# Kernel tuning notes

Hardware: AMD Instinct MI355X
Metric: run time of the kernel (lower is better)

## Reference

```python
import jax, jax.numpy as jnp
import numpy as np

N_USERS, N_ITEMS = 100000, 50000
N_EDGES, N_PAIRS = 1000000, 500000
D_IN, D_HID, D_OUT = 128, 128, 64
EPS = 1e-12


def _mean_agg(h_src, src, dst, n_dst):
    # gather src features along edges, scatter-sum to dst, divide by in-degree
    msg = h_src[src]                                            # [E, d]
    s = jax.ops.segment_sum(msg, dst, num_segments=n_dst)       # [n_dst, d]
    deg = jax.ops.segment_sum(jnp.ones(src.shape, h_src.dtype), dst, num_segments=n_dst)
    return s / jnp.maximum(deg, 1.0)[:, None]


def _conv(h_src, h_dst, src, dst, n_dst, Wn, bn, Ws, bs):
    # SAGE-mean style ConvLayer: fc_neigh(mean) + fc_self(dst), ReLU, L2 norm
    hn = _mean_agg(h_src, src, dst, n_dst)
    z = hn @ Wn + bn + h_dst @ Ws + bs
    z = jax.nn.relu(z)
    return z / jnp.maximum(jnp.linalg.norm(z, axis=-1, keepdims=True), EPS)


def _l2n(x):
    return x / jnp.maximum(jnp.linalg.norm(x, axis=-1, keepdims=True), EPS)


def setup_inputs() -> dict:
    key = jax.random.key(0)
    ks = jax.random.split(key, 20)
    f = lambda k, shp: (jax.random.normal(k, shp, jnp.float32) * 0.05)
    ri = lambda k, shp, hi: jax.random.randint(k, shp, 0, hi, jnp.int32)
    return {
        'h_user': jax.random.normal(ks[0], (N_USERS, D_IN), jnp.float32),
        'h_item': jax.random.normal(ks[1], (N_ITEMS, D_IN), jnp.float32),
        'Wn01': f(ks[2], (2, 2, D_HID, D_HID)),
        'bn01': f(ks[3], (2, 2, D_HID)),
        'Ws01': f(ks[4], (2, 2, D_HID, D_HID)),
        'bs01': f(ks[5], (2, 2, D_HID)),
        'Wn2': f(ks[6], (2, D_HID, D_OUT)),
        'bn2': f(ks[7], (2, D_OUT)),
        'Ws2': f(ks[8], (2, D_HID, D_OUT)),
        'bs2': f(ks[9], (2, D_OUT)),
        'u2i_src': ri(ks[10], (N_EDGES,), N_USERS),
        'u2i_dst': ri(ks[11], (N_EDGES,), N_ITEMS),
        'i2u_src': ri(ks[12], (N_EDGES,), N_ITEMS),
        'i2u_dst': ri(ks[13], (N_EDGES,), N_USERS),
        'pos_u': ri(ks[14], (N_PAIRS,), N_USERS),
        'pos_i': ri(ks[15], (N_PAIRS,), N_ITEMS),
        'neg_u': ri(ks[16], (N_PAIRS,), N_USERS),
        'neg_i': ri(ks[17], (N_PAIRS,), N_ITEMS),
    }


def reference(h_user, h_item, Wn01, bn01, Ws01, bs01, Wn2, bn2, Ws2, bs2,
              u2i_src, u2i_dst, i2u_src, i2u_dst, pos_u, pos_i, neg_u, neg_i):
    n_users, n_items = h_user.shape[0], h_item.shape[0]
    hu, hi = h_user, h_item
    # layers 0,1: etype 0 = user->item ('rates'), etype 1 = item->user (reverse)
    for l in range(2):
        hi_new = _conv(hu, hi, u2i_src, u2i_dst, n_items,
                       Wn01[l, 0], bn01[l, 0], Ws01[l, 0], bs01[l, 0])
        hu_new = _conv(hi, hu, i2u_src, i2u_dst, n_users,
                       Wn01[l, 1], bn01[l, 1], Ws01[l, 1], bs01[l, 1])
        hu, hi = hu_new, hi_new
    # layer 2: hidden -> out
    hi_new = _conv(hu, hi, u2i_src, u2i_dst, n_items, Wn2[0], bn2[0], Ws2[0], bs2[0])
    hu_new = _conv(hi, hu, i2u_src, i2u_dst, n_users, Wn2[1], bn2[1], Ws2[1], bs2[1])
    hu, hi = hu_new, hi_new
    # CosinePrediction on pos/neg graphs (user -rates-> item edges)
    nu, ni = _l2n(hu), _l2n(hi)
    pos_score = jnp.sum(nu[pos_u] * ni[pos_i], axis=-1)
    neg_score = jnp.sum(nu[neg_u] * ni[neg_i], axis=-1)
    return hu, hi, pos_score, neg_score
```

## Files before the change

kernel.cpp:

```cpp
#include <hip/hip_runtime.h>
#include <hip/hip_bf16.h>

#define NU 100000
#define NI 50000
#define NE 1000000
#define NP 500000

typedef unsigned short u16;
typedef unsigned int u32;
typedef __attribute__((ext_vector_type(8))) short short8;
typedef __attribute__((ext_vector_type(4))) float f32x4;

static __device__ __forceinline__ u16 f2bf(float f) {
    union { float f; u32 u; } x; x.f = f;
    u32 r = x.u + 0x7fff + ((x.u >> 16) & 1);
    return (u16)(r >> 16);
}
static __device__ __forceinline__ float bf2f(u16 h) {
    union { u32 u; float f; } x; x.u = ((u32)h) << 16;
    return x.f;
}

__global__ __launch_bounds__(256) void cvt_kernel(const float* __restrict__ in,
                                                  u16* __restrict__ out, int n8) {
    int i = blockIdx.x * blockDim.x + threadIdx.x;
    if (i >= n8) return;
    float4 a = ((const float4*)in)[2 * i];
    float4 b = ((const float4*)in)[2 * i + 1];
    ushort4 lo = {f2bf(a.x), f2bf(a.y), f2bf(a.z), f2bf(a.w)};
    ushort4 hi = {f2bf(b.x), f2bf(b.y), f2bf(b.z), f2bf(b.w)};
    ((ushort4*)out)[2 * i]     = lo;
    ((ushort4*)out)[2 * i + 1] = hi;
}

__global__ void wtrans_all_kernel(const float* __restrict__ Wn01,
                                  const float* __restrict__ Ws01,
                                  const float* __restrict__ Wn2,
                                  const float* __restrict__ Ws2,
                                  u16* __restrict__ wt) {
    int x = blockIdx.x;
    int k = threadIdx.x;
    const float *Wn, *Ws; int n, N; size_t off_out;
    if (x < 512) {
        int m = x >> 7; n = x & 127; N = 128;
        Wn = Wn01 + m * 16384; Ws = Ws01 + m * 16384;
        off_out = (size_t)m * 128 * 256;
    } else {
        int m = (x - 512) >> 6; n = (x - 512) & 63; N = 64;
        Wn = Wn2 + m * 8192; Ws = Ws2 + m * 8192;
        off_out = (size_t)4 * 128 * 256 + (size_t)m * 64 * 256;
    }
    wt[off_out + (size_t)n * 256 + k]       = f2bf(Wn[(size_t)k * N + n]);
    wt[off_out + (size_t)n * 256 + 128 + k] = f2bf(Ws[(size_t)k * N + n]);
}


__global__ void hist2_kernel(const int* __restrict__ d0, int* __restrict__ deg0,
                             int* __restrict__ rank0,
                             const int* __restrict__ d1, int* __restrict__ deg1,
                             int* __restrict__ rank1, int E) {
    int e = blockIdx.x * blockDim.x + threadIdx.x;
    if (e >= E) return;
    if (blockIdx.y == 0) {
        int d = __builtin_nontemporal_load(&d0[e]);
        int r = atomicAdd(&deg0[d], 1);
        __builtin_nontemporal_store(r, &rank0[e]);
    } else {
        int d = __builtin_nontemporal_load(&d1[e]);
        int r = atomicAdd(&deg1[d], 1);
        __builtin_nontemporal_store(r, &rank1[e]);
    }
}

__global__ void scan_local_kernel(const int* __restrict__ in, int* __restrict__ out,
                                  int* __restrict__ bsum, int n) {
    __shared__ int s[1024];
    int i = blockIdx.x * 1024 + threadIdx.x;
    int v = (i < n) ? in[i] : 0;
    s[threadIdx.x] = v;
    __syncthreads();
    for (int off = 1; off < 1024; off <<= 1) {
        int t = (threadIdx.x >= off) ? s[threadIdx.x - off] : 0;
        __syncthreads();
        s[threadIdx.x] += t;
        __syncthreads();
    }
    if (i < n) out[i] = s[threadIdx.x] - v;
    if (threadIdx.x == 1023) bsum[blockIdx.x] = s[1023];
}

__global__ void scan_bsum_kernel(int* bsum, int nb) {
    __shared__ int s[1024];
    int v = (threadIdx.x < nb) ? bsum[threadIdx.x] : 0;
    s[threadIdx.x] = v;
    __syncthreads();
    for (int off = 1; off < 1024; off <<= 1) {
        int t = (threadIdx.x >= off) ? s[threadIdx.x - off] : 0;
        __syncthreads();
        s[threadIdx.x] += t;
        __syncthreads();
    }
    if (threadIdx.x < nb) bsum[threadIdx.x] = s[threadIdx.x] - v;
}

__global__ void scan_finalize_kernel(int* __restrict__ rs, const int* __restrict__ bsum,
                                     int n, int E) {
    int i = blockIdx.x * 1024 + threadIdx.x;
    if (i < n) rs[i] += bsum[blockIdx.x];
    if (i == 0) rs[n] = E;
}

__global__ void fill2_kernel(const int* __restrict__ s0, const int* __restrict__ d0,
                             const int* __restrict__ r0, const int* __restrict__ rs0,
                             int* __restrict__ csr0,
                             const int* __restrict__ s1, const int* __restrict__ d1,
                             const int* __restrict__ r1, const int* __restrict__ rs1,
                             int* __restrict__ csr1, int E) {
    const int *src, *dst, *rk, *rs; int* csr;
    if (blockIdx.y == 0) { src = s0; dst = d0; rk = r0; rs = rs0; csr = csr0; }
    else                 { src = s1; dst = d1; rk = r1; rs = rs1; csr = csr1; }
    int e = blockIdx.x * blockDim.x + threadIdx.x;
    if (e >= E) return;
    int d = __builtin_nontemporal_load(&dst[e]);
    int r = __builtin_nontemporal_load(&rk[e]);
    int s = __builtin_nontemporal_load(&src[e]);
    csr[rs[d] + r] = s;
}

__global__ __launch_bounds__(256) void agg2_kernel(
    const u16* __restrict__ hu, const u16* __restrict__ hi,
    const int* __restrict__ rs_i, const int* __restrict__ csr_i,
    u16* __restrict__ out_i, int gi,
    const int* __restrict__ rs_u, const int* __restrict__ csr_u,
    u16* __restrict__ out_u) {
    const u16* hsrc; const int *rs, *csr; u16* out; int T, t;
    int bx = blockIdx.x;
    if (bx < gi) { hsrc = hu; rs = rs_i; csr = csr_i; out = out_i; T = NI;
                   t = bx * 4 + (threadIdx.x >> 6); }
    else         { hsrc = hi; rs = rs_u; csr = csr_u; out = out_u; T = NU;
                   t = (bx - gi) * 4 + (threadIdx.x >> 6); }
    if (t >= T) return;
    const int lane = threadIdx.x & 63;
    const int lr   = lane & 15;
    const int sub  = lane >> 4;
    int e0 = rs[t], e1 = rs[t + 1];
    float acc[8] = {};
    int e = e0 + sub;
    for (; e + 12 < e1; e += 16) {
        int s0 = __builtin_nontemporal_load(&csr[e]);
        int s1 = __builtin_nontemporal_load(&csr[e + 4]);
        int s2 = __builtin_nontemporal_load(&csr[e + 8]);
        int s3 = __builtin_nontemporal_load(&csr[e + 12]);
        short8 v0 = *(const short8*)&hsrc[(size_t)s0 * 128 + (lr << 3)];
        short8 v1 = *(const short8*)&hsrc[(size_t)s1 * 128 + (lr << 3)];
        short8 v2 = *(const short8*)&hsrc[(size_t)s2 * 128 + (lr << 3)];
        short8 v3 = *(const short8*)&hsrc[(size_t)s3 * 128 + (lr << 3)];
        #pragma unroll
        for (int q = 0; q < 8; ++q)
            acc[q] += (bf2f((u16)v0[q]) + bf2f((u16)v1[q])) +
                      (bf2f((u16)v2[q]) + bf2f((u16)v3[q]));
    }
    for (; e + 4 < e1; e += 8) {
        int s0 = __builtin_nontemporal_load(&csr[e]);
        int s1 = __builtin_nontemporal_load(&csr[e + 4]);
        short8 v0 = *(const short8*)&hsrc[(size_t)s0 * 128 + (lr << 3)];
        short8 v1 = *(const short8*)&hsrc[(size_t)s1 * 128 + (lr << 3)];
        #pragma unroll
        for (int q = 0; q < 8; ++q)
            acc[q] += bf2f((u16)v0[q]) + bf2f((u16)v1[q]);
    }
    if (e < e1) {
        int s0 = __builtin_nontemporal_load(&csr[e]);
        short8 v0 = *(const short8*)&hsrc[(size_t)s0 * 128 + (lr << 3)];
        #pragma unroll
        for (int q = 0; q < 8; ++q) acc[q] += bf2f((u16)v0[q]);
    }
    #pragma unroll
    for (int q = 0; q < 8; ++q) {
        acc[q] += __shfl_xor(acc[q], 16);
        acc[q] += __shfl_xor(acc[q], 32);
    }
    if (sub == 0) {
        float inv = (e1 > e0) ? 1.f / (float)(e1 - e0) : 0.f;
        short8 o;
        #pragma unroll
        for (int q = 0; q < 8; ++q) o[q] = (short)f2bf(acc[q] * inv);
        __builtin_nontemporal_store(o, (short8*)&out[(size_t)t * 128 + (lr << 3)]);
    }
}

template <int DOUT, bool WRITE_F32>
__global__ __launch_bounds__(256) void conv2_kernel(
    const u16* __restrict__ hn_i, const u16* __restrict__ hd_i,
    const u16* __restrict__ wt_i, const float* __restrict__ bn_i,
    const float* __restrict__ bs_i, float* __restrict__ outf_i,
    u16* __restrict__ outb_i, int ci,
    const u16* __restrict__ hn_u, const u16* __restrict__ hd_u,
    const u16* __restrict__ wt_u, const float* __restrict__ bn_u,
    const float* __restrict__ bs_u, float* __restrict__ outf_u,
    u16* __restrict__ outb_u)
{
    constexpr int NF   = DOUT / 64;
    constexpr int FSTR = (DOUT == 128) ? 132 : 68;
    __shared__ u16 smA[64 * 264];
    __shared__ float psum[4][64];
    __shared__ float sinv[64];
    float* smF = (float*)smA;

    const u16 *hn, *hd, *Wt; const float *bn, *bs; float* outf; u16* outb; int T, t0;
    if ((int)blockIdx.x < ci) {
        hn = hn_i; hd = hd_i; Wt = wt_i; bn = bn_i; bs = bs_i;
        outf = outf_i; outb = outb_i; T = NI; t0 = blockIdx.x * 64;
    } else {
        hn = hn_u; hd = hd_u; Wt = wt_u; bn = bn_u; bs = bs_u;
        outf = outf_u; outb = outb_u; T = NU; t0 = (blockIdx.x - ci) * 64;
    }

    const int tid  = threadIdx.x;
    const int wave = tid >> 6;
    const int lane = tid & 63;
    const int lr   = lane & 15;
    const int lg   = lane >> 4;

    #pragma unroll
    for (int i = 0; i < 8; ++i) {
        int lin = i * 256 + tid;
        int row = lin >> 5;
        int q   = lin & 31;
        int t   = t0 + row; if (t >= T) t = T - 1;
        const u16* srcp = (q < 16) ? &hn[(size_t)t * 128 + (q << 3)]
                                   : &hd[(size_t)t * 128 + ((q - 16) << 3)];
        *(short8*)&smA[row * 264 + (q << 3)] = *(const short8*)srcp;
    }
    __syncthreads();

    const u16* wp[NF];
    float bias[NF];
    #pragma unroll
    for (int ni = 0; ni < NF; ++ni) {
        int col = wave * (16 * NF) + ni * 16 + lr;
        wp[ni] = Wt + (size_t)col * 256;
        bias[ni] = bn[col] + bs[col];
    }

    f32x4 acc[4][NF];
    #pragma unroll
    for (int mi = 0; mi < 4; ++mi)
        #pragma unroll
        for (int ni = 0; ni < NF; ++ni)
            acc[mi][ni] = (f32x4){0.f, 0.f, 0.f, 0.f};

    #pragma unroll
    for (int ks = 0; ks < 8; ++ks) {
        const int kb = ks * 32 + (lg << 3);
        short8 b[NF];
        #pragma unroll
        for (int ni = 0; ni < NF; ++ni) b[ni] = *(const short8*)&wp[ni][kb];
        #pragma unroll
        for (int mi = 0; mi < 4; ++mi) {
            short8 a = *(const short8*)&smA[(mi * 16 + lr) * 264 + kb];
            #pragma unroll
            for (int ni = 0; ni < NF; ++ni)
                acc[mi][ni] = __builtin_amdgcn_mfma_f32_16x16x32_bf16(a, b[ni], acc[mi][ni], 0, 0, 0);
        }
    }
    __syncthreads();

    float rsum[4][4];
    #pragma unroll
    for (int mi = 0; mi < 4; ++mi) {
        #pragma unroll
        for (int j = 0; j < 4; ++j) {
            int rowg = mi * 16 + lg * 4 + j;
            float s = 0.f;
            #pragma unroll
            for (int ni = 0; ni < NF; ++ni) {
                float z = fmaxf(acc[mi][ni][j] + bias[ni], 0.f);
                int colg = wave * (16 * NF) + ni * 16 + lr;
                smF[rowg * FSTR + colg] = z;
                s = fmaf(z, z, s);
            }
            rsum[mi][j] = s;
        }
    }
    #pragma unroll
    for (int m = 1; m < 16; m <<= 1)
        #pragma unroll
        for (int mi = 0; mi < 4; ++mi)
            #pragma unroll
            for (int j = 0; j < 4; ++j)
                rsum[mi][j] += __shfl_xor(rsum[mi][j], m);
    if (lr == 0) {
        #pragma unroll
        for (int mi = 0; mi < 4; ++mi)
            #pragma unroll
            for (int j = 0; j < 4; ++j)
                psum[wave][mi * 16 + lg * 4 + j] = rsum[mi][j];
    }
    __syncthreads();
    if (tid < 64) {
        float n2 = psum[0][tid] + psum[1][tid] + psum[2][tid] + psum[3][tid];
        sinv[tid] = 1.f / fmaxf(sqrtf(n2), 1e-12f);
    }
    __syncthreads();

    constexpr int GPR  = DOUT / 8;
    constexpr int ITER = 64 * GPR / 256;
    #pragma unroll
    for (int i = 0; i < ITER; ++i) {
        int lin = i * 256 + tid;
        int row = lin / GPR, g = lin % GPR;
        int t = t0 + row;
        if (t < T) {
            float inv = sinv[row];
            float4 z0 = *(float4*)&smF[row * FSTR + g * 8];
            float4 z1 = *(float4*)&smF[row * FSTR + g * 8 + 4];
            float o0 = z0.x * inv, o1 = z0.y * inv, o2 = z0.z * inv, o3 = z0.w * inv;
            float o4 = z1.x * inv, o5 = z1.y * inv, o6 = z1.z * inv, o7 = z1.w * inv;
            short8 ob = {(short)f2bf(o0), (short)f2bf(o1), (short)f2bf(o2), (short)f2bf(o3),
                         (short)f2bf(o4), (short)f2bf(o5), (short)f2bf(o6), (short)f2bf(o7)};
            *(short8*)&outb[(size_t)t * DOUT + g * 8] = ob;
            if (WRITE_F32) {
                *(float4*)&outf[(size_t)t * DOUT + g * 8]     = (float4){o0, o1, o2, o3};
                *(float4*)&outf[(size_t)t * DOUT + g * 8 + 4] = (float4){o4, o5, o6, o7};
            }
        }
    }
}

__global__ __launch_bounds__(256) void score2_kernel(
    const u16* __restrict__ hu, const u16* __restrict__ hi,
    const int* __restrict__ pu0, const int* __restrict__ pi0, float* __restrict__ out0,
    const int* __restrict__ pu1, const int* __restrict__ pi1, float* __restrict__ out1,
    int P) {
    const int *pu, *pi; float* out;
    if (blockIdx.y == 0) { pu = pu0; pi = pi0; out = out0; }
    else                 { pu = pu1; pi = pi1; out = out1; }
    int g = threadIdx.x >> 3, l = threadIdx.x & 7;
    int p = blockIdx.x * 32 + g;
    if (p >= P) return;
    int u = __builtin_nontemporal_load(&pu[p]);
    int it = __builtin_nontemporal_load(&pi[p]);
    short8 a = *(const short8*)&hu[(size_t)u * 64 + (l << 3)];
    short8 b = *(const short8*)&hi[(size_t)it * 64 + (l << 3)];
    float d = 0.f, na = 0.f, nb = 0.f;
    #pragma unroll
    for (int q = 0; q < 8; ++q) {
        float x = bf2f((u16)a[q]), y = bf2f((u16)b[q]);
        d  = fmaf(x, y, d);
        na = fmaf(x, x, na);
        nb = fmaf(y, y, nb);
    }
    #pragma unroll
    for (int m = 1; m < 8; m <<= 1) {
        d  += __shfl_xor(d, m);
        na += __shfl_xor(na, m);
        nb += __shfl_xor(nb, m);
    }
    if (l == 0) out[p] = d / (fmaxf(sqrtf(na), 1e-12f) * fmaxf(sqrtf(nb), 1e-12f));
}


extern "C" void kernel_launch(void* const* d_in, const int* in_sizes, int n_in,
                              void* d_out, int out_size, void* d_ws, size_t ws_size,
                              hipStream_t stream) {
    const float* h_user = (const float*)d_in[0];
    const float* h_item = (const float*)d_in[1];
    const float* Wn01   = (const float*)d_in[2];
    const float* bn01   = (const float*)d_in[3];
    const float* Ws01   = (const float*)d_in[4];
    const float* bs01   = (const float*)d_in[5];
    const float* Wn2    = (const float*)d_in[6];
    const float* bn2    = (const float*)d_in[7];
    const float* Ws2    = (const float*)d_in[8];
    const float* bs2    = (const float*)d_in[9];
    const int* u2i_src  = (const int*)d_in[10];
    const int* u2i_dst  = (const int*)d_in[11];
    const int* i2u_src  = (const int*)d_in[12];
    const int* i2u_dst  = (const int*)d_in[13];
    const int* pos_u    = (const int*)d_in[14];
    const int* pos_i    = (const int*)d_in[15];
    const int* neg_u    = (const int*)d_in[16];
    const int* neg_i    = (const int*)d_in[17];

    float* out = (float*)d_out;
    float* out_hu = out;
    float* out_hi = out + (size_t)NU * 64;
    float* out_pos = out + (size_t)NU * 64 + (size_t)NI * 64;
    float* out_neg = out_pos + NP;

    char* ws = (char*)d_ws;
    size_t off = 0;
    auto alloc = [&](size_t bytes) -> void* {
        void* p = ws + off;
        off = (off + bytes + 255) & ~(size_t)255;
        return p;
    };
    u16* hu0b = (u16*)alloc((size_t)NU * 128 * 2);
    u16* hi0b = (u16*)alloc((size_t)NI * 128 * 2);
    u16* hu_b = (u16*)alloc((size_t)NU * 128 * 2);
    u16* hi_b = (u16*)alloc((size_t)NI * 128 * 2);
    u16* hu_a = (u16*)alloc((size_t)NU * 128 * 2);
    u16* hi_a = (u16*)alloc((size_t)NI * 128 * 2);
    u16* agg_i = (u16*)alloc((size_t)NI * 128 * 2);
    u16* agg_u = (u16*)alloc((size_t)NU * 128 * 2);
    u16* hu2b = (u16*)alloc((size_t)NU * 64 * 2);
    u16* hi2b = (u16*)alloc((size_t)NI * 64 * 2);
    u16* wt_all = (u16*)alloc((size_t)(4 * 128 * 256 + 2 * 64 * 256) * 2);
    u16* wt_l0_i = wt_all;
    u16* wt_l0_u = wt_all + 32768;
    u16* wt_l1_i = wt_all + 65536;
    u16* wt_l1_u = wt_all + 98304;
    u16* wt_l2_i = wt_all + 131072;
    u16* wt_l2_u = wt_all + 147456;
    int* csr_u2i = (int*)alloc((size_t)NE * 4);
    int* csr_i2u = (int*)alloc((size_t)NE * 4);
    int* rs_i   = (int*)alloc((size_t)(NI + 1) * 4);
    int* rs_u   = (int*)alloc((size_t)(NU + 1) * 4);
    int* deg    = (int*)alloc((size_t)(NI + NU) * 4);
    int* bsum   = (int*)alloc(1024 * 4);
    int* deg_i = deg, *deg_u = deg + NI;
    int* rank_i = (int*)agg_i;
    int* rank_u = (int*)agg_u;
    (void)ws_size; (void)in_sizes; (void)n_in; (void)out_size;

    const int eblocks = (NE + 255) / 256;

    cvt_kernel<<<(NU * 128 / 8 + 255) / 256, 256, 0, stream>>>(h_user, hu0b, NU * 128 / 8);
    cvt_kernel<<<(NI * 128 / 8 + 255) / 256, 256, 0, stream>>>(h_item, hi0b, NI * 128 / 8);
    wtrans_all_kernel<<<640, 128, 0, stream>>>(Wn01, Ws01, Wn2, Ws2, wt_all);

    hipMemsetAsync(deg, 0, (size_t)(NI + NU) * 4, stream);
    hist2_kernel<<<dim3(eblocks, 2), 256, 0, stream>>>(u2i_dst, deg_i, rank_i,
                                                       i2u_dst, deg_u, rank_u, NE);
    {
        int nb = (NI + 1023) / 1024;
        scan_local_kernel<<<nb, 1024, 0, stream>>>(deg_i, rs_i, bsum, NI);
        scan_bsum_kernel<<<1, 1024, 0, stream>>>(bsum, nb);
        scan_finalize_kernel<<<nb, 1024, 0, stream>>>(rs_i, bsum, NI, NE);
    }
    {
        int nb = (NU + 1023) / 1024;
        scan_local_kernel<<<nb, 1024, 0, stream>>>(deg_u, rs_u, bsum, NU);
        scan_bsum_kernel<<<1, 1024, 0, stream>>>(bsum, nb);
        scan_finalize_kernel<<<nb, 1024, 0, stream>>>(rs_u, bsum, NU, NE);
    }
    fill2_kernel<<<dim3(eblocks, 2), 256, 0, stream>>>(
        u2i_src, u2i_dst, rank_i, rs_i, csr_u2i,
        i2u_src, i2u_dst, rank_u, rs_u, csr_i2u, NE);

    const int gi = (NI + 3) / 4, gu = (NU + 3) / 4;
    const int ci = (NI + 63) / 64, cu = (NU + 63) / 64;

    agg2_kernel<<<gi + gu, 256, 0, stream>>>(hu0b, hi0b, rs_i, csr_u2i, agg_i, gi,
                                             rs_u, csr_i2u, agg_u);
    conv2_kernel<128, false><<<ci + cu, 256, 0, stream>>>(
        agg_i, hi0b, wt_l0_i, bn01 + 0, bs01 + 0, nullptr, hi_b, ci,
        agg_u, hu0b, wt_l0_u, bn01 + 128, bs01 + 128, nullptr, hu_b);
    agg2_kernel<<<gi + gu, 256, 0, stream>>>(hu_b, hi_b, rs_i, csr_u2i, agg_i, gi,
                                             rs_u, csr_i2u, agg_u);
    conv2_kernel<128, false><<<ci + cu, 256, 0, stream>>>(
        agg_i, hi_b, wt_l1_i, bn01 + 256, bs01 + 256, nullptr, hi_a, ci,
        agg_u, hu_b, wt_l1_u, bn01 + 384, bs01 + 384, nullptr, hu_a);
    agg2_kernel<<<gi + gu, 256, 0, stream>>>(hu_a, hi_a, rs_i, csr_u2i, agg_i, gi,
                                             rs_u, csr_i2u, agg_u);
    conv2_kernel<64, true><<<ci + cu, 256, 0, stream>>>(
        agg_i, hi_a, wt_l2_i, bn2 + 0, bs2 + 0, out_hi, hi2b, ci,
        agg_u, hu_a, wt_l2_u, bn2 + 64, bs2 + 64, out_hu, hu2b);

    score2_kernel<<<dim3((NP + 31) / 32, 2), 256, 0, stream>>>(
        hu2b, hi2b, pos_u, pos_i, out_pos, neg_u, neg_i, out_neg, NP);
}
```

Baseline: 569.3 us.

## Project before aggregation in final layer to halve gather width

For the last layer, features are projected first with a combined 128x128 weight (neighbor half and self half), then the 64-wide neighbor projection is mean-aggregated, since mean aggregation commutes with the linear map. This halves the bytes gathered per edge in the third aggregation, at the cost of an extra projection kernel and a separate combine/normalize kernel. The agg grid is also interleaved between item and user blocks, and the two CSR scans are merged into dual-launch kernels to cut launch count.

Result: slower. 581.9 us (+2.2%).

```diff
diff --git a/kernel.cpp b/kernel.cpp
--- a/kernel.cpp
+++ b/kernel.cpp
@@ -5,6 +5,10 @@
 #define NI 50000
 #define NE 1000000
 #define NP 500000
+
+#define GIB 12500
+#define GUB 25000
+#define AGG_GRID 50000
 
 typedef unsigned short u16;
 typedef unsigned int u32;
@@ -40,18 +44,24 @@
                                   u16* __restrict__ wt) {
     int x = blockIdx.x;
     int k = threadIdx.x;
-    const float *Wn, *Ws; int n, N; size_t off_out;
     if (x < 512) {
-        int m = x >> 7; n = x & 127; N = 128;
-        Wn = Wn01 + m * 16384; Ws = Ws01 + m * 16384;
-        off_out = (size_t)m * 128 * 256;
+        int m = x >> 7, n = x & 127;
+        const float* Wn = Wn01 + m * 16384;
+        const float* Ws = Ws01 + m * 16384;
+        size_t o = (size_t)m * 128 * 256;
+        wt[o + (size_t)n * 256 + k]       = f2bf(Wn[(size_t)k * 128 + n]);
+        wt[o + (size_t)n * 256 + 128 + k] = f2bf(Ws[(size_t)k * 128 + n]);
     } else {
-        int m = (x - 512) >> 6; n = (x - 512) & 63; N = 64;
-        Wn = Wn2 + m * 8192; Ws = Ws2 + m * 8192;
-        off_out = (size_t)4 * 128 * 256 + (size_t)m * 64 * 256;
-    }
-    wt[off_out + (size_t)n * 256 + k]       = f2bf(Wn[(size_t)k * N + n]);
-    wt[off_out + (size_t)n * 256 + 128 + k] = f2bf(Ws[(size_t)k * N + n]);
+        int m = (x - 512) >> 7;
+        int n = (x - 512) & 127;
+        size_t o = 131072 + (size_t)m * 16384;
+        float v;
+        if (m == 0) v = (n < 64) ? Wn2[(size_t)k * 64 + n]
+                                 : Ws2[8192 + (size_t)k * 64 + (n - 64)];
+        else        v = (n < 64) ? Wn2[8192 + (size_t)k * 64 + n]
+                                 : Ws2[(size_t)k * 64 + (n - 64)];
+        wt[o + (size_t)n * 128 + k] = f2bf(v);
+    }
 }
 
 
@@ -72,8 +82,13 @@
     }
 }
 
-__global__ void scan_local_kernel(const int* __restrict__ in, int* __restrict__ out,
-                                  int* __restrict__ bsum, int n) {
+__global__ void scan2_local_kernel(const int* __restrict__ in0, int* __restrict__ out0,
+                                   int* __restrict__ bsum0, int n0,
+                                   const int* __restrict__ in1, int* __restrict__ out1,
+                                   int* __restrict__ bsum1, int n1) {
+    const int* in; int *out, *bsum; int n;
+    if (blockIdx.y == 0) { in = in0; out = out0; bsum = bsum0; n = n0; }
+    else                 { in = in1; out = out1; bsum = bsum1; n = n1; }
     __shared__ int s[1024];
     int i = blockIdx.x * 1024 + threadIdx.x;
     int v = (i < n) ? in[i] : 0;
@@ -89,9 +104,12 @@
     if (threadIdx.x == 1023) bsum[blockIdx.x] = s[1023];
 }
 
-__global__ void scan_bsum_kernel(int* bsum, int nb) {
+__global__ void scan2_bsum_kernel(int* b0, int nb0, int* b1, int nb1) {
+    int* bsum; int nb;
+    if (blockIdx.y == 0) { bsum = b0; nb = nb0; }
+    else                 { bsum = b1; nb = nb1; }
     __shared__ int s[1024];
-    int v = (threadIdx.x < nb) ? bsum[threadIdx.x] : 0;
+    int v = ((int)threadIdx.x < nb) ? bsum[threadIdx.x] : 0;
     s[threadIdx.x] = v;
     __syncthreads();
     for (int off = 1; off < 1024; off <<= 1) {
@@ -100,11 +118,15 @@
         s[threadIdx.x] += t;
         __syncthreads();
     }
-    if (threadIdx.x < nb) bsum[threadIdx.x] = s[threadIdx.x] - v;
-}
-
-__global__ void scan_finalize_kernel(int* __restrict__ rs, const int* __restrict__ bsum,
-                                     int n, int E) {
+    if ((int)threadIdx.x < nb) bsum[threadIdx.x] = s[threadIdx.x] - v;
+}
+
+__global__ void scan2_finalize_kernel(int* __restrict__ rs0, const int* __restrict__ b0,
+                                      int n0, int* __restrict__ rs1,
+                                      const int* __restrict__ b1, int n1, int E) {
+    int* rs; const int* bsum; int n;
+    if (blockIdx.y == 0) { rs = rs0; bsum = b0; n = n0; }
+    else                 { rs = rs1; bsum = b1; n = n1; }
     int i = blockIdx.x * 1024 + threadIdx.x;
     if (i < n) rs[i] += bsum[blockIdx.x];
     if (i == 0) rs[n] = E;
@@ -130,15 +152,18 @@
 __global__ __launch_bounds__(256) void agg2_kernel(
     const u16* __restrict__ hu, const u16* __restrict__ hi,
     const int* __restrict__ rs_i, const int* __restrict__ csr_i,
-    u16* __restrict__ out_i, int gi,
+    u16* __restrict__ out_i,
     const int* __restrict__ rs_u, const int* __restrict__ csr_u,
     u16* __restrict__ out_u) {
-    const u16* hsrc; const int *rs, *csr; u16* out; int T, t;
-    int bx = blockIdx.x;
-    if (bx < gi) { hsrc = hu; rs = rs_i; csr = csr_i; out = out_i; T = NI;
-                   t = bx * 4 + (threadIdx.x >> 6); }
-    else         { hsrc = hi; rs = rs_u; csr = csr_u; out = out_u; T = NU;
-                   t = (bx - gi) * 4 + (threadIdx.x >> 6); }
+    const u16* hsrc; const int *rs, *csr; u16* out; int T, blk;
+    int base = blockIdx.x >> 3, r8 = blockIdx.x & 7;
+    if (r8 < 4) { blk = base * 4 + r8;
+                  if (blk >= GIB) return;
+                  hsrc = hu; rs = rs_i; csr = csr_i; out = out_i; T = NI; }
+    else        { blk = base * 4 + (r8 - 4);
+                  if (blk >= GUB) return;
+                  hsrc = hi; rs = rs_u; csr = csr_u; out = out_u; T = NU; }
+    int t = blk * 4 + (threadIdx.x >> 6);
     if (t >= T) return;
     const int lane = threadIdx.x & 63;
     const int lr   = lane & 15;
@@ -189,31 +214,80 @@
     }
 }
 
-template <int DOUT, bool WRITE_F32>
+__global__ __launch_bounds__(256) void agg64_kernel(
+    const u16* __restrict__ pu, const u16* __restrict__ pi,
+    const int* __restrict__ rs_i, const int* __restrict__ csr_i,
+    u16* __restrict__ out_i,
+    const int* __restrict__ rs_u, const int* __restrict__ csr_u,
+    u16* __restrict__ out_u) {
+    const u16* hsrc; const int *rs, *csr; u16* out; int T, blk;
+    int base = blockIdx.x >> 3, r8 = blockIdx.x & 7;
+    if (r8 < 4) { blk = base * 4 + r8;
+                  if (blk >= GIB) return;
+                  hsrc = pu; rs = rs_i; csr = csr_i; out = out_i; T = NI; }
+    else        { blk = base * 4 + (r8 - 4);
+                  if (blk >= GUB) return;
+                  hsrc = pi; rs = rs_u; csr = csr_u; out = out_u; T = NU; }
+    int t = blk * 4 + (threadIdx.x >> 6);
+    if (t >= T) return;
+    const int lane = threadIdx.x & 63;
+    const int lr   = lane & 7;
+    const int sub  = lane >> 3;
+    int e0 = rs[t], e1 = rs[t + 1];
+    float acc[8] = {};
+    int e = e0 + sub;
+    for (; e + 8 < e1; e += 16) {
+        int s0 = __builtin_nontemporal_load(&csr[e]);
+        int s1 = __builtin_nontemporal_load(&csr[e + 8]);
+        short8 v0 = *(const short8*)&hsrc[(size_t)s0 * 128 + (lr << 3)];
+        short8 v1 = *(const short8*)&hsrc[(size_t)s1 * 128 + (lr << 3)];
+        #pragma unroll
+        for (int q = 0; q < 8; ++q)
+            acc[q] += bf2f((u16)v0[q]) + bf2f((u16)v1[q]);
+    }
+    if (e < e1) {
+        int s0 = __builtin_nontemporal_load(&csr[e]);
+        short8 v0 = *(const short8*)&hsrc[(size_t)s0 * 128 + (lr << 3)];
+        #pragma unroll
+        for (int q = 0; q < 8; ++q) acc[q] += bf2f((u16)v0[q]);
+    }
+    #pragma unroll
+    for (int q = 0; q < 8; ++q) {
+        acc[q] += __shfl_xor(acc[q], 8);
+        acc[q] += __shfl_xor(acc[q], 16);
+        acc[q] += __shfl_xor(acc[q], 32);
+    }
+    if (sub == 0) {
+        float inv = (e1 > e0) ? 1.f / (float)(e1 - e0) : 0.f;
+        short8 o;
+        #pragma unroll
+        for (int q = 0; q < 8; ++q) o[q] = (short)f2bf(acc[q] * inv);
+        __builtin_nontemporal_store(o, (short8*)&out[(size_t)t * 64 + (lr << 3)]);
+    }
+}
+
 __global__ __launch_bounds__(256) void conv2_kernel(
     const u16* __restrict__ hn_i, const u16* __restrict__ hd_i,
     const u16* __restrict__ wt_i, const float* __restrict__ bn_i,
-    const float* __restrict__ bs_i, float* __restrict__ outf_i,
-    u16* __restrict__ outb_i, int ci,
+    const float* __restrict__ bs_i, u16* __restrict__ outb_i, int ci,
     const u16* __restrict__ hn_u, const u16* __restrict__ hd_u,
     const u16* __restrict__ wt_u, const float* __restrict__ bn_u,
-    const float* __restrict__ bs_u, float* __restrict__ outf_u,
-    u16* __restrict__ outb_u)
+    const float* __restrict__ bs_u, u16* __restrict__ outb_u)
 {
-    constexpr int NF   = DOUT / 64;
-    constexpr int FSTR = (DOUT == 128) ? 132 : 68;
+    constexpr int NF   = 2;
+    constexpr int FSTR = 132;
     __shared__ u16 smA[64 * 264];
     __shared__ float psum[4][64];
     __shared__ float sinv[64];
     float* smF = (float*)smA;
 
-    const u16 *hn, *hd, *Wt; const float *bn, *bs; float* outf; u16* outb; int T, t0;
+    const u16 *hn, *hd, *Wt; const float *bn, *bs; u16* outb; int T, t0;
     if ((int)blockIdx.x < ci) {
         hn = hn_i; hd = hd_i; Wt = wt_i; bn = bn_i; bs = bs_i;
-        outf = outf_i; outb = outb_i; T = NI; t0 = blockIdx.x * 64;
+        outb = outb_i; T = NI; t0 = blockIdx.x * 64;
     } else {
         hn = hn_u; hd = hd_u; Wt = wt_u; bn = bn_u; bs = bs_u;
-        outf = outf_u; outb = outb_u; T = NU; t0 = (blockIdx.x - ci) * 64;
+        outb = outb_u; T = NU; t0 = (blockIdx.x - ci) * 64;
     }
 
     const int tid  = threadIdx.x;
@@ -238,7 +312,7 @@
     float bias[NF];
     #pragma unroll
     for (int ni = 0; ni < NF; ++ni) {
-        int col = wave * (16 * NF) + ni * 16 + lr;
+        int col = wave * 32 + ni * 16 + lr;
         wp[ni] = Wt + (size_t)col * 256;
         bias[ni] = bn[col] + bs[col];
     }
@@ -276,7 +350,7 @@
             #pragma unroll
             for (int ni = 0; ni < NF; ++ni) {
                 float z = fmaxf(acc[mi][ni][j] + bias[ni], 0.f);
-                int colg = wave * (16 * NF) + ni * 16 + lr;
+                int colg = wave * 32 + ni * 16 + lr;
                 smF[rowg * FSTR + colg] = z;
                 s = fmaf(z, z, s);
             }
@@ -304,28 +378,159 @@
     }
     __syncthreads();
 
-    constexpr int GPR  = DOUT / 8;
-    constexpr int ITER = 64 * GPR / 256;
-    #pragma unroll
-    for (int i = 0; i < ITER; ++i) {
+    #pragma unroll
+    for (int i = 0; i < 4; ++i) {
         int lin = i * 256 + tid;
-        int row = lin / GPR, g = lin % GPR;
+        int row = lin >> 4, g = lin & 15;
         int t = t0 + row;
         if (t < T) {
             float inv = sinv[row];
             float4 z0 = *(float4*)&smF[row * FSTR + g * 8];
             float4 z1 = *(float4*)&smF[row * FSTR + g * 8 + 4];
-            float o0 = z0.x * inv, o1 = z0.y * inv, o2 = z0.z * inv, o3 = z0.w * inv;
-            float o4 = z1.x * inv, o5 = z1.y * inv, o6 = z1.z * inv, o7 = z1.w * inv;
-            short8 ob = {(short)f2bf(o0), (short)f2bf(o1), (short)f2bf(o2), (short)f2bf(o3),
-                         (short)f2bf(o4), (short)f2bf(o5), (short)f2bf(o6), (short)f2bf(o7)};
-            *(short8*)&outb[(size_t)t * DOUT + g * 8] = ob;
-            if (WRITE_F32) {
-                *(float4*)&outf[(size_t)t * DOUT + g * 8]     = (float4){o0, o1, o2, o3};
-                *(float4*)&outf[(size_t)t * DOUT + g * 8 + 4] = (float4){o4, o5, o6, o7};
-            }
+            short8 ob = {(short)f2bf(z0.x * inv), (short)f2bf(z0.y * inv),
+                         (short)f2bf(z0.z * inv), (short)f2bf(z0.w * inv),
+                         (short)f2bf(z1.x * inv), (short)f2bf(z1.y * inv),
+                         (short)f2bf(z1.z * inv), (short)f2bf(z1.w * inv)};
+            *(short8*)&outb[(size_t)t * 128 + g * 8] = ob;
         }
     }
+}
+
+__global__ __launch_bounds__(256) void proj2_kernel(
+    const u16* __restrict__ A_i, const u16* __restrict__ wt_pi,
+    u16* __restrict__ out_i, int ci,
+    const u16* __restrict__ A_u, const u16* __restrict__ wt_pu,
+    u16* __restrict__ out_u)
+{
+    constexpr int NF = 2;
+    constexpr int FSTR = 132;
+    __shared__ float smF[64 * FSTR];
+    u16* smA = (u16*)smF;
+
+    const u16 *A, *Wt; u16* outb; int T, t0;
+    if ((int)blockIdx.x < ci) {
+        A = A_i; Wt = wt_pi; outb = out_i; T = NI; t0 = blockIdx.x * 64;
+    } else {
+        A = A_u; Wt = wt_pu; outb = out_u; T = NU; t0 = (blockIdx.x - ci) * 64;
+    }
+
+    const int tid  = threadIdx.x;
+    const int wave = tid >> 6;
+    const int lane = tid & 63;
+    const int lr   = lane & 15;
+    const int lg   = lane >> 4;
+
+    #pragma unroll
+    for (int i = 0; i < 4; ++i) {
+        int lin = i * 256 + tid;
+        int row = lin >> 4;
+        int q   = lin & 15;
+        int t   = t0 + row; if (t >= T) t = T - 1;
+        *(short8*)&smA[row * 136 + (q << 3)] =
+            *(const short8*)&A[(size_t)t * 128 + (q << 3)];
+    }
+    __syncthreads();
+
+    const u16* wp[NF];
+    #pragma unroll
+    for (int ni = 0; ni < NF; ++ni) {
+        int col = wave * 32 + ni * 16 + lr;
+        wp[ni] = Wt + (size_t)col * 128;
+    }
+
+    f32x4 acc[4][NF];
+    #pragma unroll
+    for (int mi = 0; mi < 4; ++mi)
+        #pragma unroll
+        for (int ni = 0; ni < NF; ++ni)
+            acc[mi][ni] = (f32x4){0.f, 0.f, 0.f, 0.f};
+
+    #pragma unroll
+    for (int ks = 0; ks < 4; ++ks) {
+        const int kb = ks * 32 + (lg << 3);
+        short8 b[NF];
+        #pragma unroll
+        for (int ni = 0; ni < NF; ++ni) b[ni] = *(const short8*)&wp[ni][kb];
+        #pragma unroll
+        for (int mi = 0; mi < 4; ++mi) {
+            short8 a = *(const short8*)&smA[(mi * 16 + lr) * 136 + kb];
+            #pragma unroll
+            for (int ni = 0; ni < NF; ++ni)
+                acc[mi][ni] = __builtin_amdgcn_mfma_f32_16x16x32_bf16(a, b[ni], acc[mi][ni], 0, 0, 0);
+        }
+    }
+    __syncthreads();
+
+    #pragma unroll
+    for (int mi = 0; mi < 4; ++mi)
+        #pragma unroll
+        for (int j = 0; j < 4; ++j) {
+            int rowg = mi * 16 + lg * 4 + j;
+            #pragma unroll
+            for (int ni = 0; ni < NF; ++ni)
+                smF[rowg * FSTR + wave * 32 + ni * 16 + lr] = acc[mi][ni][j];
+        }
+    __syncthreads();
+
+    #pragma unroll
+    for (int i = 0; i < 4; ++i) {
+        int lin = i * 256 + tid;
+        int row = lin >> 4, g = lin & 15;
+        int t = t0 + row;
+        if (t < T) {
+            float4 z0 = *(float4*)&smF[row * FSTR + g * 8];
+            float4 z1 = *(float4*)&smF[row * FSTR + g * 8 + 4];
+            short8 ob = {(short)f2bf(z0.x), (short)f2bf(z0.y),
+                         (short)f2bf(z0.z), (short)f2bf(z0.w),
+                         (short)f2bf(z1.x), (short)f2bf(z1.y),
+                         (short)f2bf(z1.z), (short)f2bf(z1.w)};
+            *(short8*)&outb[(size_t)t * 128 + g * 8] = ob;
+        }
+    }
+}
+
+__global__ __launch_bounds__(256) void combine2_kernel(
+    const u16* __restrict__ agg_i, const u16* __restrict__ proj_i,
+    const float* __restrict__ bn2, const float* __restrict__ bs2,
+    float* __restrict__ outf_i, u16* __restrict__ outb_i, int cbi,
+    const u16* __restrict__ agg_u, const u16* __restrict__ proj_u,
+    float* __restrict__ outf_u, u16* __restrict__ outb_u)
+{
+    const u16 *agg, *proj; const float *bn, *bs; float* outf; u16* outb; int T, r0;
+    if ((int)blockIdx.x < cbi) {
+        agg = agg_i; proj = proj_i; bn = bn2;      bs = bs2;
+        outf = outf_i; outb = outb_i; T = NI; r0 = blockIdx.x * 32;
+    } else {
+        agg = agg_u; proj = proj_u; bn = bn2 + 64; bs = bs2 + 64;
+        outf = outf_u; outb = outb_u; T = NU; r0 = (blockIdx.x - cbi) * 32;
+    }
+    int g = threadIdx.x >> 3, l = threadIdx.x & 7;
+    int r = r0 + g;
+    if (r >= T) return;
+    short8 va = *(const short8*)&agg[(size_t)r * 64 + (l << 3)];
+    short8 vs = *(const short8*)&proj[(size_t)r * 128 + 64 + (l << 3)];
+    float z[8];
+    float s = 0.f;
+    #pragma unroll
+    for (int q = 0; q < 8; ++q) {
+        float v = bf2f((u16)va[q]) + bf2f((u16)vs[q]) + bn[l * 8 + q] + bs[l * 8 + q];
+        v = fmaxf(v, 0.f);
+        z[q] = v;
+        s = fmaf(v, v, s);
+    }
+    s += __shfl_xor(s, 1);
+    s += __shfl_xor(s, 2);
+    s += __shfl_xor(s, 4);
+    float inv = 1.f / fmaxf(sqrtf(s), 1e-12f);
+    short8 ob;
+    float4 o0, o1;
+    o0.x = z[0] * inv; o0.y = z[1] * inv; o0.z = z[2] * inv; o0.w = z[3] * inv;
+    o1.x = z[4] * inv; o1.y = z[5] * inv; o1.z = z[6] * inv; o1.w = z[7] * inv;
+    #pragma unroll
+    for (int q = 0; q < 8; ++q) ob[q] = (short)f2bf(z[q] * inv);
+    *(short8*)&outb[(size_t)r * 64 + (l << 3)] = ob;
+    *(float4*)&outf[(size_t)r * 64 + (l << 3)]     = o0;
+    *(float4*)&outf[(size_t)r * 64 + (l << 3) + 4] = o1;
 }
 
 __global__ __launch_bounds__(256) void score2_kernel(
@@ -406,67 +611,69 @@
     u16* agg_u = (u16*)alloc((size_t)NU * 128 * 2);
     u16* hu2b = (u16*)alloc((size_t)NU * 64 * 2);
     u16* hi2b = (u16*)alloc((size_t)NI * 64 * 2);
-    u16* wt_all = (u16*)alloc((size_t)(4 * 128 * 256 + 2 * 64 * 256) * 2);
+    u16* wt_all = (u16*)alloc((size_t)(4 * 128 * 256 + 2 * 128 * 128) * 2);
     u16* wt_l0_i = wt_all;
     u16* wt_l0_u = wt_all + 32768;
     u16* wt_l1_i = wt_all + 65536;
     u16* wt_l1_u = wt_all + 98304;
-    u16* wt_l2_i = wt_all + 131072;
-    u16* wt_l2_u = wt_all + 147456;
+    u16* wt_pu   = wt_all + 131072;
+    u16* wt_pi   = wt_all + 147456;
     int* csr_u2i = (int*)alloc((size_t)NE * 4);
     int* csr_i2u = (int*)alloc((size_t)NE * 4);
     int* rs_i   = (int*)alloc((size_t)(NI + 1) * 4);
     int* rs_u   = (int*)alloc((size_t)(NU + 1) * 4);
     int* deg    = (int*)alloc((size_t)(NI + NU) * 4);
-    int* bsum   = (int*)alloc(1024 * 4);
+    int* bsum_i = (int*)alloc(1024 * 4);
+    int* bsum_u = (int*)alloc(1024 * 4);
     int* deg_i = deg, *deg_u = deg + NI;
     int* rank_i = (int*)agg_i;
     int* rank_u = (int*)agg_u;
+    u16* proj_u = hu_b;
+    u16* proj_i = hi_b;
+    u16* agg64_i = agg_i;
+    u16* agg64_u = agg_u;
     (void)ws_size; (void)in_sizes; (void)n_in; (void)out_size;
 
     const int eblocks = (NE + 255) / 256;
 
     cvt_kernel<<<(NU * 128 / 8 + 255) / 256, 256, 0, stream>>>(h_user, hu0b, NU * 128 / 8);
     cvt_kernel<<<(NI * 128 / 8 + 255) / 256, 256, 0, stream>>>(h_item, hi0b, NI * 128 / 8);
-    wtrans_all_kernel<<<640, 128, 0, stream>>>(Wn01, Ws01, Wn2, Ws2, wt_all);
+    wtrans_all_kernel<<<768, 128, 0, stream>>>(Wn01, Ws01, Wn2, Ws2, wt_all);
 
     hipMemsetAsync(deg, 0, (size_t)(NI + NU) * 4, stream);
     hist2_kernel<<<dim3(eblocks, 2), 256, 0, stream>>>(u2i_dst, deg_i, rank_i,
                                                        i2u_dst, deg_u, rank_u, NE);
-    {
-        int nb = (NI + 1023) / 1024;
-        scan_local_kernel<<<nb, 1024, 0, stream>>>(deg_i, rs_i, bsum, NI);
-        scan_bsum_kernel<<<1, 1024, 0, stream>>>(bsum, nb);
-        scan_finalize_kernel<<<nb, 1024, 0, stream>>>(rs_i, bsum, NI, NE);
-    }
-    {
-        int nb = (NU + 1023) / 1024;
-        scan_local_kernel<<<nb, 1024, 0, stream>>>(deg_u, rs_u, bsum, NU);
-        scan_bsum_kernel<<<1, 1024, 0, stream>>>(bsum, nb);
-        scan_finalize_kernel<<<nb, 1024, 0, stream>>>(rs_u, bsum, NU, NE);
-    }
+    const int nb_i = (NI + 1023) / 1024, nb_u = (NU + 1023) / 1024;
+    const int nb_max = (nb_i > nb_u) ? nb_i : nb_u;
+    scan2_local_kernel<<<dim3(nb_max, 2), 1024, 0, stream>>>(
+        deg_i, rs_i, bsum_i, NI, deg_u, rs_u, bsum_u, NU);
+    scan2_bsum_kernel<<<dim3(1, 2), 1024, 0, stream>>>(bsum_i, nb_i, bsum_u, nb_u);
+    scan2_finalize_kernel<<<dim3(nb_max, 2), 1024, 0, stream>>>(
+        rs_i, bsum_i, NI, rs_u, bsum_u, NU, NE);
     fill2_kernel<<<dim3(eblocks, 2), 256, 0, stream>>>(
         u2i_src, u2i_dst, rank_i, rs_i, csr_u2i,
         i2u_src, i2u_dst, rank_u, rs_u, csr_i2u, NE);
 
-    const int gi = (NI + 3) / 4, gu = (NU + 3) / 4;
     const int ci = (NI + 63) / 64, cu = (NU + 63) / 64;
-
-    agg2_kernel<<<gi + gu, 256, 0, stream>>>(hu0b, hi0b, rs_i, csr_u2i, agg_i, gi,
-                                             rs_u, csr_i2u, agg_u);
-    conv2_kernel<128, false><<<ci + cu, 256, 0, stream>>>(
-        agg_i, hi0b, wt_l0_i, bn01 + 0, bs01 + 0, nullptr, hi_b, ci,
-        agg_u, hu0b, wt_l0_u, bn01 + 128, bs01 + 128, nullptr, hu_b);
-    agg2_kernel<<<gi + gu, 256, 0, stream>>>(hu_b, hi_b, rs_i, csr_u2i, agg_i, gi,
-                                             rs_u, csr_i2u, agg_u);
-    conv2_kernel<128, false><<<ci + cu, 256, 0, stream>>>(
-        agg_i, hi_b, wt_l1_i, bn01 + 256, bs01 + 256, nullptr, hi_a, ci,
-        agg_u, hu_b, wt_l1_u, bn01 + 384, bs01 + 384, nullptr, hu_a);
-    agg2_kernel<<<gi + gu, 256, 0, stream>>>(hu_a, hi_a, rs_i, csr_u2i, agg_i, gi,
-                                             rs_u, csr_i2u, agg_u);
-    conv2_kernel<64, true><<<ci + cu, 256, 0, stream>>>(
-        agg_i, hi_a, wt_l2_i, bn2 + 0, bs2 + 0, out_hi, hi2b, ci,
-        agg_u, hu_a, wt_l2_u, bn2 + 64, bs2 + 64, out_hu, hu2b);
+    const int cbi = (NI + 31) / 32, cbu = (NU + 31) / 32;
+
+    agg2_kernel<<<AGG_GRID, 256, 0, stream>>>(hu0b, hi0b, rs_i, csr_u2i, agg_i,
+                                              rs_u, csr_i2u, agg_u);
+    conv2_kernel<<<ci + cu, 256, 0, stream>>>(
+        agg_i, hi0b, wt_l0_i, bn01 + 0, bs01 + 0, hi_b, ci,
+        agg_u, hu0b, wt_l0_u, bn01 + 128, bs01 + 128, hu_b);
+    agg2_kernel<<<AGG_GRID, 256, 0, stream>>>(hu_b, hi_b, rs_i, csr_u2i, agg_i,
+                                              rs_u, csr_i2u, agg_u);
+    conv2_kernel<<<ci + cu, 256, 0, stream>>>(
+        agg_i, hi_b, wt_l1_i, bn01 + 256, bs01 + 256, hi_a, ci,
+        agg_u, hu_b, wt_l1_u, bn01 + 384, bs01 + 384, hu_a);
+    proj2_kernel<<<ci + cu, 256, 0, stream>>>(hi_a, wt_pi, proj_i, ci,
+                                              hu_a, wt_pu, proj_u);
+    agg64_kernel<<<AGG_GRID, 256, 0, stream>>>(proj_u, proj_i, rs_i, csr_u2i, agg64_i,
+                                               rs_u, csr_i2u, agg64_u);
+    combine2_kernel<<<cbi + cbu, 256, 0, stream>>>(
+        agg64_i, proj_i, bn2, bs2, out_hi, hi2b, cbi,
+        agg64_u, proj_u, out_hu, hu2b);
 
     score2_kernel<<<dim3((NP + 31) / 32, 2), 256, 0, stream>>>(
         hu2b, hi2b, pos_u, pos_i, out_pos, neg_u, neg_i, out_neg, NP);
```
